# Performance work log

Measured on AMD Instinct MI355X. Metric: run time of the kernel, lower is better.

The kernel has to match this reference:

```python
import jax, jax.numpy as jnp
import numpy as np

IN_N, IN_D, OUT_N, OUT_D = 2048, 16, 64, 16
LN_EPS = 1e-5

def setup_inputs() -> dict:
    key = jax.random.key(0)
    k1, k2 = jax.random.split(key)
    w_const = np.sqrt(OUT_N / (IN_D * IN_N)).astype(np.float32)
    return {
        "input": jax.random.normal(k1, (128, IN_N, IN_D), dtype=jnp.float32),
        "w": w_const * jax.random.normal(k2, (IN_N, IN_D, OUT_N, OUT_D), dtype=jnp.float32),
        "ln_gamma": jnp.ones((OUT_D,), dtype=jnp.float32),
        "ln_beta": jnp.zeros((OUT_D,), dtype=jnp.float32),
    }

def _squash(x):
    # squash along last dim: (|x|^2/(1+|x|^2)) * x/|x|
    sq = jnp.sum(x * x, axis=-1, keepdims=True)
    return (sq / (1.0 + sq)) * x / jnp.sqrt(sq)

def reference(input, w, ln_gamma, ln_beta):
    b, n, a = input.shape
    m = w.shape[2]
    # query_key=None path: softmax over zeros -> uniform 1/m routing coeffs
    qk = jnp.full((n, m), 1.0 / m, dtype=input.dtype)
    # bmd = sum_{n,a} qk[n,m] * input[b,n,a] * w[n,a,m,d]
    v = jnp.einsum('nm,bna,namd->bmd', qk, input, w)
    v = _squash(v)
    new_qk = jnp.einsum('bna,namd,bmd->bnm', input, w, v)
    # dropout with p=0 (eval) is identity; LayerNorm over out_d_capsules
    mu = jnp.mean(v, axis=-1, keepdims=True)
    var = jnp.mean((v - mu) ** 2, axis=-1, keepdims=True)
    v = (v - mu) / jnp.sqrt(var + LN_EPS) * ln_gamma + ln_beta
    return (new_qk, v)
```

## Files before the change

kernel.cpp:

```cpp
#include <hip/hip_runtime.h>
#include <cstdint>
#include <cstddef>

typedef short bfrag __attribute__((ext_vector_type(8)));
typedef float facc  __attribute__((ext_vector_type(4)));

namespace {
constexpr int B = 128, N = 2048, A = 16, M = 64, D = 16;
constexpr int NA = N * A;
constexpr int MD = M * D;
constexpr size_t C_ELEMS = (size_t)B * MD;
}

static __device__ __forceinline__ ushort f2bf(float x) {
    uint u = __float_as_uint(x);
    u += 0x7fffu + ((u >> 16) & 1u);
    return (ushort)(u >> 16);
}
static __device__ __forceinline__ bfrag ld_frag16(const ushort* p) {
    union { uint4 q; bfrag v; } u;
    u.q = *(const uint4*)p;
    return u.v;
}
static __device__ __forceinline__ bfrag ld_frag4(const ushort* p) {
    const uint* q = (const uint*)p;
    union { uint a[4]; bfrag v; } u;
    u.a[0] = q[0]; u.a[1] = q[1]; u.a[2] = q[2]; u.a[3] = q[3];
    return u.v;
}

__global__ __launch_bounds__(512, 2) void k1_mfma(const float* __restrict__ in,
                                                  const float* __restrict__ w,
                                                  float* __restrict__ part,
                                                  int nch) {
    const int mdg   = blockIdx.x;
    const int chunk = blockIdx.y;
    const int t     = threadIdx.x;
    const int nap   = NA / nch;
    const int nkt   = nap / 64;
    __shared__ __align__(16) ushort in_t[128 * 72];
    __shared__ __align__(16) ushort w_t[256 * 66];
    const int wv = t >> 6, tl = t & 63;
    const int wb = wv >> 2, wm = wv & 3;
    const int lr = tl & 15, hi = tl >> 4;

    facc acc[4][4];
    #pragma unroll
    for (int i = 0; i < 4; ++i)
        #pragma unroll
        for (int j = 0; j < 4; ++j) acc[i][j] = facc{0.f, 0.f, 0.f, 0.f};

    float4 pin[4], pw[8];
    const int ib  = t >> 4, ik = t & 15;
    const int wk  = t >> 6, wmd = t & 63;

    int na0 = (size_t)chunk * nap;
    #pragma unroll
    for (int q = 0; q < 4; ++q)
        pin[q] = *(const float4*)(in + (size_t)(q * 32 + ib) * NA + na0 + ik * 4);
    #pragma unroll
    for (int q = 0; q < 8; ++q)
        pw[q] = *(const float4*)(w + (size_t)(na0 + q * 8 + wk) * MD + mdg * 256 + wmd * 4);

    for (int kt = 0; kt < nkt; ++kt) {
        __syncthreads();
        #pragma unroll
        for (int q = 0; q < 4; ++q) {
            union { ushort s[4]; uint2 u; } pk;
            pk.s[0] = f2bf(pin[q].x); pk.s[1] = f2bf(pin[q].y);
            pk.s[2] = f2bf(pin[q].z); pk.s[3] = f2bf(pin[q].w);
            *(uint2*)(&in_t[(q * 32 + ib) * 72 + ik * 4]) = pk.u;
        }
        #pragma unroll
        for (int q = 0; q < 8; ++q) {
            const int krow = q * 8 + wk;
            w_t[(wmd * 4 + 0) * 66 + krow] = f2bf(pw[q].x);
            w_t[(wmd * 4 + 1) * 66 + krow] = f2bf(pw[q].y);
            w_t[(wmd * 4 + 2) * 66 + krow] = f2bf(pw[q].z);
            w_t[(wmd * 4 + 3) * 66 + krow] = f2bf(pw[q].w);
        }
        __syncthreads();
        if (kt + 1 < nkt) {
            const int nan = na0 + 64;
            #pragma unroll
            for (int q = 0; q < 4; ++q)
                pin[q] = *(const float4*)(in + (size_t)(q * 32 + ib) * NA + nan + ik * 4);
            #pragma unroll
            for (int q = 0; q < 8; ++q)
                pw[q] = *(const float4*)(w + (size_t)(nan + q * 8 + wk) * MD + mdg * 256 + wmd * 4);
        }
        #pragma unroll
        for (int ks = 0; ks < 2; ++ks) {
            bfrag af[4], bf[4];
            #pragma unroll
            for (int bt = 0; bt < 4; ++bt)
                af[bt] = ld_frag16(&in_t[(wb * 64 + bt * 16 + lr) * 72 + ks * 32 + hi * 8]);
            #pragma unroll
            for (int mt = 0; mt < 4; ++mt)
                bf[mt] = ld_frag4(&w_t[(wm * 64 + mt * 16 + lr) * 66 + ks * 32 + hi * 8]);
            #pragma unroll
            for (int bt = 0; bt < 4; ++bt)
                #pragma unroll
                for (int mt = 0; mt < 4; ++mt)
                    acc[bt][mt] = __builtin_amdgcn_mfma_f32_16x16x32_bf16(
                        af[bt], bf[mt], acc[bt][mt], 0, 0, 0);
        }
        na0 += 64;
    }
    #pragma unroll
    for (int bt = 0; bt < 4; ++bt)
        #pragma unroll
        for (int mt = 0; mt < 4; ++mt) {
            const int b  = wb * 64 + bt * 16 + hi * 4;
            const int md = mdg * 256 + wm * 64 + mt * 16 + lr;
            #pragma unroll
            for (int r = 0; r < 4; ++r)
                part[((size_t)chunk * B + b + r) * MD + md] = acc[bt][mt][r];
        }
}

__global__ __launch_bounds__(256) void k2_squash_ln(const float* __restrict__ part,
                                                    const float* __restrict__ gamma,
                                                    const float* __restrict__ beta,
                                                    float* __restrict__ v_sq,
                                                    float* __restrict__ out_v,
                                                    int nch) {
    const int idx = blockIdx.x * 256 + threadIdx.x;
    const int d   = idx & 15;
    float s = 0.f;
    for (int c = 0; c < nch; ++c) s += part[(size_t)c * C_ELEMS + idx];
    const float v = s * (1.0f / 64.0f);
    float sq = v * v;
    #pragma unroll
    for (int off = 1; off < 16; off <<= 1) sq += __shfl_xor(sq, off, 16);
    const float f  = sqrtf(sq) / (1.0f + sq);
    const float vs = v * f;
    v_sq[idx] = vs;
    float mu = vs;
    #pragma unroll
    for (int off = 1; off < 16; off <<= 1) mu += __shfl_xor(mu, off, 16);
    mu *= (1.0f / 16.0f);
    const float dd = vs - mu;
    float var = dd * dd;
    #pragma unroll
    for (int off = 1; off < 16; off <<= 1) var += __shfl_xor(var, off, 16);
    var *= (1.0f / 16.0f);
    out_v[idx] = dd / sqrtf(var + 1e-5f) * gamma[d] + beta[d];
}

__global__ __launch_bounds__(512, 2) void k3_mfma(const float* __restrict__ in,
                                                  const float* __restrict__ w,
                                                  const float* __restrict__ vsq,
                                                  float* __restrict__ qk) {
    const int mg = blockIdx.x, seg = blockIdx.y;
    const int m0 = mg * 16, n0 = seg * 16;
    const int t  = threadIdx.x;
    const int wv = t >> 6, tl = t & 63;
    const int lr = tl & 15, hi = tl >> 4;
    const int bb = wv * 16 + lr;
    __shared__ __align__(16) ushort wt3[2][16 * 392];
    __shared__ __align__(16) ushort inb[2][128 * 24];

    float vsr[16][4];
    #pragma unroll
    for (int mi = 0; mi < 16; ++mi) {
        const float4 v = *(const float4*)(vsq + ((size_t)bb * M + m0 + mi) * D + hi * 4);
        vsr[mi][0] = v.x; vsr[mi][1] = v.y; vsr[mi][2] = v.z; vsr[mi][3] = v.w;
    }
    const int sa = t >> 6, smd = t & 63;
    const int mloc = smd >> 2, d0 = (smd & 3) * 4;
    const int sb = t >> 2, saf = t & 3;
    float4 pw0, pw1, pinr;
    const int koff = (hi < 2) ? hi * 8 : 0;

    auto ldg = [&](int n) {
        pw0  = *(const float4*)(w + (size_t)(n * 16 + sa) * MD + m0 * 16 + smd * 4);
        pw1  = *(const float4*)(w + (size_t)(n * 16 + sa + 8) * MD + m0 * 16 + smd * 4);
        pinr = *(const float4*)(in + (size_t)sb * NA + n * 16 + saf * 4);
    };
    auto stg = [&](int p) {
        ushort* wb_ = &wt3[p][mloc * 392];
        wb_[(d0 + 0) * 24 + sa] = f2bf(pw0.x);
        wb_[(d0 + 1) * 24 + sa] = f2bf(pw0.y);
        wb_[(d0 + 2) * 24 + sa] = f2bf(pw0.z);
        wb_[(d0 + 3) * 24 + sa] = f2bf(pw0.w);
        wb_[(d0 + 0) * 24 + sa + 8] = f2bf(pw1.x);
        wb_[(d0 + 1) * 24 + sa + 8] = f2bf(pw1.y);
        wb_[(d0 + 2) * 24 + sa + 8] = f2bf(pw1.z);
        wb_[(d0 + 3) * 24 + sa + 8] = f2bf(pw1.w);
        union { ushort s[4]; uint2 u; } pk;
        pk.s[0] = f2bf(pinr.x); pk.s[1] = f2bf(pinr.y);
        pk.s[2] = f2bf(pinr.z); pk.s[3] = f2bf(pinr.w);
        *(uint2*)(&inb[p][sb * 24 + saf * 4]) = pk.u;
    };

    ldg(n0);
    stg(0);
    __syncthreads();
    for (int i = 0; i < 16; ++i) {
        const int n = n0 + i, p = i & 1;
        if (i + 1 < 16) ldg(n0 + i + 1);
        uint4 braw = *(const uint4*)(&inb[p][bb * 24 + koff]);
        if (hi >= 2) { braw.x = 0u; braw.y = 0u; braw.z = 0u; braw.w = 0u; }
        union { uint4 q; bfrag v; } bu; bu.q = braw;
        const bfrag binf = bu.v;
        float qk_[4];
        const facc zero = facc{0.f, 0.f, 0.f, 0.f};
        #pragma unroll
        for (int mi = 0; mi < 16; ++mi) {
            uint4 araw = *(const uint4*)(&wt3[p][mi * 392 + lr * 24 + koff]);
            if (hi >= 2) { araw.x = 0u; araw.y = 0u; araw.z = 0u; araw.w = 0u; }
            union { uint4 q; bfrag v; } au; au.q = araw;
            const facc c = __builtin_amdgcn_mfma_f32_16x16x32_bf16(au.v, binf, zero, 0, 0, 0);
            float r0 = c[0] * vsr[mi][0] + c[1] * vsr[mi][1]
                     + c[2] * vsr[mi][2] + c[3] * vsr[mi][3];
            r0 += __shfl_xor(r0, 16);
            r0 += __shfl_xor(r0, 32);
            qk_[mi & 3] = (hi == (mi >> 2)) ? r0 : qk_[mi & 3];
        }
        const float4 o = {qk_[0], qk_[1], qk_[2], qk_[3]};
        *(float4*)(qk + ((size_t)bb * N + n) * M + m0 + hi * 4) = o;
        __syncthreads();
        if (i + 1 < 16) { stg((i + 1) & 1); __syncthreads(); }
    }
}

extern "C" void kernel_launch(void* const* d_in, const int* in_sizes, int n_in,
                              void* d_out, int out_size, void* d_ws, size_t ws_size,
                              hipStream_t stream) {
    const float* in    = (const float*)d_in[0];
    const float* w     = (const float*)d_in[1];
    const float* gamma = (const float*)d_in[2];
    const float* beta  = (const float*)d_in[3];
    float* out_qk = (float*)d_out;
    float* out_v  = out_qk + (size_t)B * N * M;

    int nch = 64;
    if (ws_size < (64 + 1) * C_ELEMS * sizeof(float)) nch = 16;
    if (ws_size < (16 + 1) * C_ELEMS * sizeof(float)) nch = 8;
    float* part = (float*)d_ws;
    float* vsq  = part + (size_t)nch * C_ELEMS;

    k1_mfma<<<dim3(4, nch), 512, 0, stream>>>(in, w, part, nch);
    k2_squash_ln<<<(int)(C_ELEMS / 256), 256, 0, stream>>>(part, gamma, beta, vsq, out_v, nch);
    k3_mfma<<<dim3(4, 128), 512, 0, stream>>>(in, w, vsq, out_qk);
}
```

Before: 125.9 us.

## Swizzle LDS tiles in qk MFMA kernel and drop redundant barrier

Replaces the padded shared-memory layout for the bf16 weight and input tiles with a compact layout that uses an XOR swizzle, which cuts LDS footprint and targets bank conflicts on the fragment reads. Global-to-register weight loads are remapped to match the new layout. The barrier between the MFMA compute and the staging of the next buffer is removed, relying on double buffering so only one sync per iteration remains. The risk is bank conflicts on the scattered 16-bit stores into the swizzled layout, and correctness depends on the double-buffer ordering.

After: 146.9 us. 16.6% more time.

```diff
diff --git a/kernel.cpp b/kernel.cpp
--- a/kernel.cpp
+++ b/kernel.cpp
@@ -152,76 +152,79 @@
                                                   const float* __restrict__ w,
                                                   const float* __restrict__ vsq,
                                                   float* __restrict__ qk) {
-    const int mg = blockIdx.x, seg = blockIdx.y;
-    const int m0 = mg * 16, n0 = seg * 16;
+    const int m0 = blockIdx.x * 16;
+    const int n0 = blockIdx.y * 16;
     const int t  = threadIdx.x;
     const int wv = t >> 6, tl = t & 63;
     const int lr = tl & 15, hi = tl >> 4;
-    const int bb = wv * 16 + lr;
-    __shared__ __align__(16) ushort wt3[2][16 * 392];
-    __shared__ __align__(16) ushort inb[2][128 * 24];
-
-    float vsr[16][4];
-    #pragma unroll
-    for (int mi = 0; mi < 16; ++mi) {
-        const float4 v = *(const float4*)(vsq + ((size_t)bb * M + m0 + mi) * D + hi * 4);
-        vsr[mi][0] = v.x; vsr[mi][1] = v.y; vsr[mi][2] = v.z; vsr[mi][3] = v.w;
-    }
-    const int sa = t >> 6, smd = t & 63;
-    const int mloc = smd >> 2, d0 = (smd & 3) * 4;
-    const int sb = t >> 2, saf = t & 3;
-    float4 pw0, pw1, pinr;
-    const int koff = (hi < 2) ? hi * 8 : 0;
-
+    const int b  = wv * 16 + lr;
+    __shared__ __align__(16) ushort w_t[2][4096];
+    __shared__ __align__(16) ushort in_t[2][2048];
+
+    float4 vsr[16];
+    #pragma unroll
+    for (int mi = 0; mi < 16; ++mi)
+        vsr[mi] = *(const float4*)(vsq + ((size_t)b * M + m0 + mi) * D + hi * 4);
+
+    float4 pw[2], pin;
     auto ldg = [&](int n) {
-        pw0  = *(const float4*)(w + (size_t)(n * 16 + sa) * MD + m0 * 16 + smd * 4);
-        pw1  = *(const float4*)(w + (size_t)(n * 16 + sa + 8) * MD + m0 * 16 + smd * 4);
-        pinr = *(const float4*)(in + (size_t)sb * NA + n * 16 + saf * 4);
+        #pragma unroll
+        for (int q = 0; q < 2; ++q) {
+            const int idx = q * 512 + t;
+            const int a = idx >> 6, mloc = (idx >> 2) & 15, d4 = idx & 3;
+            pw[q] = *(const float4*)(
+                w + (((size_t)n * A + a) * M + m0 + mloc) * D + d4 * 4);
+        }
+        pin = *(const float4*)(in + (size_t)(t >> 2) * NA + n * A + (t & 3) * 4);
     };
     auto stg = [&](int p) {
-        ushort* wb_ = &wt3[p][mloc * 392];
-        wb_[(d0 + 0) * 24 + sa] = f2bf(pw0.x);
-        wb_[(d0 + 1) * 24 + sa] = f2bf(pw0.y);
-        wb_[(d0 + 2) * 24 + sa] = f2bf(pw0.z);
-        wb_[(d0 + 3) * 24 + sa] = f2bf(pw0.w);
-        wb_[(d0 + 0) * 24 + sa + 8] = f2bf(pw1.x);
-        wb_[(d0 + 1) * 24 + sa + 8] = f2bf(pw1.y);
-        wb_[(d0 + 2) * 24 + sa + 8] = f2bf(pw1.z);
-        wb_[(d0 + 3) * 24 + sa + 8] = f2bf(pw1.w);
+        #pragma unroll
+        for (int q = 0; q < 2; ++q) {
+            const int idx = q * 512 + t;
+            const int a = idx >> 6, mloc = (idx >> 2) & 15, d4 = idx & 3;
+            const int base = mloc * 256 + (a >> 3) * 128 + (a & 7);
+            const int swz  = (mloc & 7) << 3;
+            w_t[p][(base + (d4 * 4 + 0) * 8) ^ swz] = f2bf(pw[q].x);
+            w_t[p][(base + (d4 * 4 + 1) * 8) ^ swz] = f2bf(pw[q].y);
+            w_t[p][(base + (d4 * 4 + 2) * 8) ^ swz] = f2bf(pw[q].z);
+            w_t[p][(base + (d4 * 4 + 3) * 8) ^ swz] = f2bf(pw[q].w);
+        }
         union { ushort s[4]; uint2 u; } pk;
-        pk.s[0] = f2bf(pinr.x); pk.s[1] = f2bf(pinr.y);
-        pk.s[2] = f2bf(pinr.z); pk.s[3] = f2bf(pinr.w);
-        *(uint2*)(&inb[p][sb * 24 + saf * 4]) = pk.u;
+        pk.s[0] = f2bf(pin.x); pk.s[1] = f2bf(pin.y);
+        pk.s[2] = f2bf(pin.z); pk.s[3] = f2bf(pin.w);
+        *(uint2*)(&in_t[p][(t >> 2) * 16 + (t & 3) * 4]) = pk.u;
     };
 
     ldg(n0);
     stg(0);
     __syncthreads();
     for (int i = 0; i < 16; ++i) {
-        const int n = n0 + i, p = i & 1;
+        const int p = i & 1;
         if (i + 1 < 16) ldg(n0 + i + 1);
-        uint4 braw = *(const uint4*)(&inb[p][bb * 24 + koff]);
+        uint4 braw = *(const uint4*)&in_t[p][b * 16 + (hi & 1) * 8];
         if (hi >= 2) { braw.x = 0u; braw.y = 0u; braw.z = 0u; braw.w = 0u; }
         union { uint4 q; bfrag v; } bu; bu.q = braw;
-        const bfrag binf = bu.v;
-        float qk_[4];
         const facc zero = facc{0.f, 0.f, 0.f, 0.f};
+        float out4[4];
         #pragma unroll
         for (int mi = 0; mi < 16; ++mi) {
-            uint4 araw = *(const uint4*)(&wt3[p][mi * 392 + lr * 24 + koff]);
+            const int ridx = (mi * 256 + (hi & 1) * 128 + lr * 8) ^ ((mi & 7) << 3);
+            uint4 araw = *(const uint4*)&w_t[p][ridx];
             if (hi >= 2) { araw.x = 0u; araw.y = 0u; araw.z = 0u; araw.w = 0u; }
             union { uint4 q; bfrag v; } au; au.q = araw;
-            const facc c = __builtin_amdgcn_mfma_f32_16x16x32_bf16(au.v, binf, zero, 0, 0, 0);
-            float r0 = c[0] * vsr[mi][0] + c[1] * vsr[mi][1]
-                     + c[2] * vsr[mi][2] + c[3] * vsr[mi][3];
-            r0 += __shfl_xor(r0, 16);
-            r0 += __shfl_xor(r0, 32);
-            qk_[mi & 3] = (hi == (mi >> 2)) ? r0 : qk_[mi & 3];
-        }
-        const float4 o = {qk_[0], qk_[1], qk_[2], qk_[3]};
-        *(float4*)(qk + ((size_t)bb * N + n) * M + m0 + hi * 4) = o;
-        __syncthreads();
-        if (i + 1 < 16) { stg((i + 1) & 1); __syncthreads(); }
+            const facc c = __builtin_amdgcn_mfma_f32_16x16x32_bf16(au.v, bu.v, zero, 0, 0, 0);
+            float s = c[0] * vsr[mi].x + c[1] * vsr[mi].y
+                    + c[2] * vsr[mi].z + c[3] * vsr[mi].w;
+            s += __shfl_xor(s, 16);
+            s += __shfl_xor(s, 32);
+            if ((mi >> 2) == hi) out4[mi & 3] = s;
+        }
+        const float4 o = {out4[0], out4[1], out4[2], out4[3]};
+        *(float4*)(qk + ((size_t)b * N + n0 + i) * M + m0 + hi * 4) = o;
+        if (i + 1 < 16) {
+            stg(p ^ 1);
+            __syncthreads();
+        }
     }
 }
 
```
